# Kernel tuning notes

Hardware: AMD Instinct MI355X
Metric: run time of the kernel (lower is better)

## Reference

```python
import jax, jax.numpy as jnp
import numpy as np

DIM, NH, NL, NP, HD, FF = 256, 8, 4, 4, 32, 1024
LN_EPS = 1e-5


def _ln(x, w, b):
    m = jnp.mean(x, axis=-1, keepdims=True)
    v = jnp.mean((x - m) ** 2, axis=-1, keepdims=True)
    return (x - m) * jax.lax.rsqrt(v + LN_EPS) * w + b


def _sample_level(value_l, loc, H, W):
    # value_l: (B, H*W, nH, hd) ; loc: (B, Lq, nH, P, 2) normalized coords in [0,1]
    B, Lq, nH, P, _ = loc.shape
    # grid_sample(align_corners=False): pixel coord = norm * size - 0.5
    x = loc[..., 0] * W - 0.5
    y = loc[..., 1] * H - 0.5
    x0 = jnp.floor(x)
    y0 = jnp.floor(y)
    wx1 = x - x0
    wy1 = y - y0
    wx0 = 1.0 - wx1
    wy0 = 1.0 - wy1
    x0i = x0.astype(jnp.int32)
    y0i = y0.astype(jnp.int32)

    def corner(xi, yi, w):
        valid = ((xi >= 0) & (xi < W) & (yi >= 0) & (yi < H)).astype(value_l.dtype)
        idx = jnp.clip(yi, 0, H - 1) * W + jnp.clip(xi, 0, W - 1)
        idx = idx.transpose(0, 1, 3, 2).reshape(B, Lq * P, nH, 1)  # per-head gather index
        v = jnp.take_along_axis(value_l, idx, axis=1).reshape(B, Lq, P, nH, -1)
        wm = (w * valid).transpose(0, 1, 3, 2)[..., None]  # (B,Lq,P,nH,1)
        return v * wm

    return (corner(x0i, y0i, wx0 * wy0) + corner(x0i + 1, y0i, wx1 * wy0)
            + corner(x0i, y0i + 1, wx0 * wy1) + corner(x0i + 1, y0i + 1, wx1 * wy1))


def _msdeform_attn(q, value, ref, shapes_np, starts_np, W_off, b_off, W_attn, b_attn):
    B, S, _ = q.shape
    off = (q @ W_off + b_off).reshape(B, S, NH, NL, NP, 2)
    attn = jax.nn.softmax((q @ W_attn + b_attn).reshape(B, S, NH, NL * NP), axis=-1)
    attn = attn.reshape(B, S, NH, NL, NP)
    # offset normalizer is (W, H) per level
    norm = jnp.asarray(shapes_np[:, ::-1].copy(), dtype=q.dtype)  # (NL, 2)
    loc = ref[:, :, None, :, None, :] + off / norm[None, None, None, :, None, :]
    outs = []
    for l in range(NL):
        H, W = int(shapes_np[l, 0]), int(shapes_np[l, 1])
        s = int(starts_np[l])
        vl = value[:, s:s + H * W]  # (B, H*W, NH, HD)
        outs.append(_sample_level(vl, loc[:, :, :, l], H, W))  # (B,S,P,NH,HD)
    samp = jnp.stack(outs, axis=2)  # (B,S,NL,P,NH,HD)
    w = attn.transpose(0, 1, 3, 4, 2)[..., None]  # (B,S,NL,P,NH,1)
    return (samp * w).sum(axis=(2, 3)).reshape(B, S, NH * HD)


def setup_inputs() -> dict:
    key = jax.random.key(0)
    ks = jax.random.split(key, 16)
    shapes = np.array([[64, 64], [32, 32], [16, 16], [8, 8]], dtype=np.int64)
    starts = np.array([0, 4096, 5120, 5376], dtype=np.int64)
    B, S = 4, 5440
    std = 0.02
    return {
        "input": jax.random.normal(ks[0], (B, S, DIM), jnp.float32),
        "pos": jax.random.normal(ks[1], (B, S, DIM), jnp.float32),
        "reference_point": jax.random.uniform(ks[2], (B, S, NL, 2), jnp.float32),
        "shape": shapes,
        "level_start": starts,
        "ln1_w": jnp.ones((DIM,), jnp.float32),
        "ln1_b": jnp.zeros((DIM,), jnp.float32),
        "W_off": jax.random.normal(ks[3], (DIM, NH * NL * NP * 2), jnp.float32) * std,
        "b_off": jax.random.normal(ks[4], (NH * NL * NP * 2,), jnp.float32) * 0.1,
        "W_attn": jax.random.normal(ks[5], (DIM, NH * NL * NP), jnp.float32) * std,
        "b_attn": jnp.zeros((NH * NL * NP,), jnp.float32),
        "W_val": jax.random.normal(ks[6], (DIM, DIM), jnp.float32) * std,
        "b_val": jnp.zeros((DIM,), jnp.float32),
        "W_out": jax.random.normal(ks[7], (DIM, DIM), jnp.float32) * std,
        "b_out": jnp.zeros((DIM,), jnp.float32),
        "ln2_w": jnp.ones((DIM,), jnp.float32),
        "ln2_b": jnp.zeros((DIM,), jnp.float32),
        "ff_w1": jax.random.normal(ks[8], (DIM, FF), jnp.float32) * std,
        "ff_b1": jnp.zeros((FF,), jnp.float32),
        "ff_w2": jax.random.normal(ks[9], (FF, DIM), jnp.float32) * std,
        "ff_b2": jnp.zeros((DIM,), jnp.float32),
    }


def reference(input, pos, reference_point, shape, level_start,
              ln1_w, ln1_b, W_off, b_off, W_attn, b_attn, W_val, b_val,
              W_out, b_out, ln2_w, ln2_b, ff_w1, ff_b1, ff_w2, ff_b2):
    shapes_np = np.asarray(shape)
    starts_np = np.asarray(level_start)
    B, S, _ = input.shape
    # pre-norm query with positional embedding
    q = _ln(input, ln1_w, ln1_b) + pos
    # value projection acts on the raw residual stream (input_flatten)
    value = (input @ W_val + b_val).reshape(B, S, NH, HD)
    attn_out = _msdeform_attn(q, value, reference_point, shapes_np, starts_np,
                              W_off, b_off, W_attn, b_attn) @ W_out + b_out
    x = input + attn_out  # dropout is identity in eval
    y = _ln(x, ln2_w, ln2_b)
    ff = jax.nn.relu(y @ ff_w1 + ff_b1) @ ff_w2 + ff_b2
    return x + ff
```

## Files before the change

### kernel.cpp

```cpp
#include <hip/hip_runtime.h>
#include <hip/hip_fp16.h>
#include <math.h>

#define DIM 256
#define NHEAD 8
#define NLVL 4
#define NPT 4
#define HDIM 32
#define FFDIM 1024
#define BATCH 4
#define SEQ 5440
#define MTOK (BATCH * SEQ)

typedef __attribute__((ext_vector_type(8))) short short8;
typedef __attribute__((ext_vector_type(4))) float f32x4;

__device__ __forceinline__ unsigned short f2bf(float f) {
    union { float f; unsigned int u; } x; x.f = f;
    unsigned int r = x.u + 0x7fffu + ((x.u >> 16) & 1u);
    return (unsigned short)(r >> 16);
}

__device__ __forceinline__ void gll16(const unsigned short* g, unsigned short* l) {
    __builtin_amdgcn_global_load_lds(
        (const __attribute__((address_space(1))) void*)g,
        (__attribute__((address_space(3))) void*)l,
        16, 0, 0);
}

__global__ __launch_bounds__(256) void wtprep_kernel(
    const float* __restrict__ W_val, const float* __restrict__ W_off,
    const float* __restrict__ W_attn, const float* __restrict__ W_out,
    const float* __restrict__ ff_w1, const float* __restrict__ ff_w2,
    const float* __restrict__ b_off, const float* __restrict__ b_attn,
    unsigned short* __restrict__ wts, float* __restrict__ bcomb)
{
    int idx = blockIdx.x * 256 + threadIdx.x;
    if (blockIdx.x == 0 && threadIdx.x < 384) {
        int li = threadIdx.x;
        bcomb[li] = (li < 256) ? b_off[li] : b_attn[li - 256];
    }
    const float* W; int K, N, base;
    if      (idx < 65536)  { W = W_val;  K = 256;  N = 256;  base = 0; }
    else if (idx < 131072) { W = W_off;  K = 256;  N = 256;  base = 65536; }
    else if (idx < 163840) { W = W_attn; K = 256;  N = 128;  base = 131072; }
    else if (idx < 229376) { W = W_out;  K = 256;  N = 256;  base = 163840; }
    else if (idx < 491520) { W = ff_w1;  K = 256;  N = 1024; base = 229376; }
    else if (idx < 753664) { W = ff_w2;  K = 1024; N = 256;  base = 491520; }
    else return;
    int li = idx - base;
    int k = li % K;
    int n = li / K;
    wts[idx] = f2bf(W[(size_t)k * N + n]);
}

template<int COPY_BF16>
__global__ __launch_bounds__(256) void ln_kernel(
    const float* __restrict__ x, const float* __restrict__ w,
    const float* __restrict__ bvec, const float* __restrict__ addend,
    unsigned short* __restrict__ out, unsigned short* __restrict__ xbf)
{
    int wv = threadIdx.x >> 6, lane = threadIdx.x & 63;
    int token = blockIdx.x * 4 + wv;
    size_t base = (size_t)token * DIM + lane * 4;
    float4 v = *(const float4*)(x + base);
    float s  = v.x + v.y + v.z + v.w;
    float s2 = v.x * v.x + v.y * v.y + v.z * v.z + v.w * v.w;
    #pragma unroll
    for (int o = 1; o < 64; o <<= 1) {
        s  += __shfl_xor(s, o);
        s2 += __shfl_xor(s2, o);
    }
    float m  = s * (1.0f / DIM);
    float rs = rsqrtf(s2 * (1.0f / DIM) - m * m + 1e-5f);
    float4 w4 = *(const float4*)(w + lane * 4);
    float4 b4 = *(const float4*)(bvec + lane * 4);
    float4 r;
    r.x = (v.x - m) * rs * w4.x + b4.x;
    r.y = (v.y - m) * rs * w4.y + b4.y;
    r.z = (v.z - m) * rs * w4.z + b4.z;
    r.w = (v.w - m) * rs * w4.w + b4.w;
    if (addend) {
        float4 a = *(const float4*)(addend + base);
        r.x += a.x; r.y += a.y; r.z += a.z; r.w += a.w;
    }
    ushort4 o4;
    o4.x = f2bf(r.x); o4.y = f2bf(r.y); o4.z = f2bf(r.z); o4.w = f2bf(r.w);
    *(ushort4*)(out + base) = o4;
    if (COPY_BF16) {
        ushort4 c;
        c.x = f2bf(v.x); c.y = f2bf(v.y); c.z = f2bf(v.z); c.w = f2bf(v.w);
        *(ushort4*)(xbf + base) = c;
    }
}

template<int K, int OUT, int RELU, int HAS_RES>
__global__ __launch_bounds__(256) void mfma_gemm(
    const unsigned short* __restrict__ A,
    const unsigned short* __restrict__ Bt,
    const float* __restrict__ bias,
    const float* __restrict__ res,
    void* __restrict__ Cout,
    int M, int N)
{
    __shared__ __align__(16) unsigned short As[128 * 32];
    __shared__ __align__(16) unsigned short Bs[128 * 32];

    const int tid  = threadIdx.x;
    const int lane = tid & 63;
    const int wv   = tid >> 6;
    const int wr   = wv >> 1;
    const int wc   = wv & 1;
    const int m16  = lane & 15;
    const int quad = lane >> 4;

    const int bm0 = blockIdx.y * 128;
    const int bn0 = blockIdx.x * 128;

    const int e0 = wv * 1024 + lane * 8;
    const int e1 = e0 + 512;
    const int r0 = e0 >> 5, c0 = e0 & 31;
    const int r1 = e1 >> 5, c1 = e1 & 31;

    f32x4 acc[4][4] = {};

    for (int k0 = 0; k0 < K; k0 += 32) {
        if (k0) __syncthreads();
        gll16(A  + (size_t)(bm0 + r0) * K + k0 + c0, As + e0);
        gll16(A  + (size_t)(bm0 + r1) * K + k0 + c1, As + e1);
        gll16(Bt + (size_t)(bn0 + r0) * K + k0 + c0, Bs + e0);
        gll16(Bt + (size_t)(bn0 + r1) * K + k0 + c1, Bs + e1);
        __syncthreads();

        short8 af[4], bf[4];
        #pragma unroll
        for (int i = 0; i < 4; i++)
            af[i] = *(const short8*)&As[(wr * 64 + i * 16 + m16) * 32 + quad * 8];
        #pragma unroll
        for (int j = 0; j < 4; j++)
            bf[j] = *(const short8*)&Bs[(wc * 64 + j * 16 + m16) * 32 + quad * 8];

        #pragma unroll
        for (int i = 0; i < 4; i++)
            #pragma unroll
            for (int j = 0; j < 4; j++)
                acc[i][j] = __builtin_amdgcn_mfma_f32_16x16x32_bf16(
                    bf[j], af[i], acc[i][j], 0, 0, 0);
    }

    float4 bias4[4];
    #pragma unroll
    for (int j = 0; j < 4; j++)
        bias4[j] = *(const float4*)(bias + bn0 + wc * 64 + j * 16 + quad * 4);

    #pragma unroll
    for (int i = 0; i < 4; i++) {
        int row = bm0 + wr * 64 + i * 16 + m16;
        #pragma unroll
        for (int j = 0; j < 4; j++) {
            int col = bn0 + wc * 64 + j * 16 + quad * 4;
            float v0 = acc[i][j][0] + bias4[j].x;
            float v1 = acc[i][j][1] + bias4[j].y;
            float v2 = acc[i][j][2] + bias4[j].z;
            float v3 = acc[i][j][3] + bias4[j].w;
            if (HAS_RES) {
                float4 rr = *(const float4*)(res + (size_t)row * N + col);
                v0 += rr.x; v1 += rr.y; v2 += rr.z; v3 += rr.w;
            }
            if (RELU) {
                v0 = fmaxf(v0, 0.0f); v1 = fmaxf(v1, 0.0f);
                v2 = fmaxf(v2, 0.0f); v3 = fmaxf(v3, 0.0f);
            }
            if (OUT == 0) {
                float4 o = {v0, v1, v2, v3};
                *(float4*)((float*)Cout + (size_t)row * N + col) = o;
            } else if (OUT == 1) {
                ushort4 o;
                o.x = f2bf(v0); o.y = f2bf(v1); o.z = f2bf(v2); o.w = f2bf(v3);
                *(ushort4*)((unsigned short*)Cout + (size_t)row * N + col) = o;
            } else {
                ushort4 o;
                o.x = __half_as_ushort(__float2half_rn(v0));
                o.y = __half_as_ushort(__float2half_rn(v1));
                o.z = __half_as_ushort(__float2half_rn(v2));
                o.w = __half_as_ushort(__float2half_rn(v3));
                *(ushort4*)((unsigned short*)Cout + (size_t)row * N + col) = o;
            }
        }
    }
}

__global__ __launch_bounds__(256) void msdeform_kernel(
    const unsigned short* __restrict__ value_h,
    const float* __restrict__ oa,
    const float* __restrict__ ref,
    unsigned short* __restrict__ samp_out)
{
    const int Hs[NLVL] = {64, 32, 16, 8};
    const int Ws[NLVL] = {64, 32, 16, 8};
    const int St[NLVL] = {0, 4096, 5120, 5376};

    const int t  = threadIdx.x;
    const int tt = t >> 5;
    const int rr = t & 31;
    const int h  = rr >> 2;
    const int q  = rr & 3;
    const int token = blockIdx.x * 8 + tt;
    const int b = token / SEQ;

    __shared__ float s_attn[8][8][17];
    __shared__ uint2 s_tab[8][8][65];

    const float* oat = oa + (size_t)token * 384;
    float4 a4 = *(const float4*)(oat + 256 + h * 16 + q * 4);
    s_attn[tt][h][q * 4 + 0] = a4.x;
    s_attn[tt][h][q * 4 + 1] = a4.y;
    s_attn[tt][h][q * 4 + 2] = a4.z;
    s_attn[tt][h][q * 4 + 3] = a4.w;
    float4 o0 = *(const float4*)(oat + h * 32 + q * 8);
    float4 o1 = *(const float4*)(oat + h * 32 + q * 8 + 4);
    float2 rf = *(const float2*)(ref + (size_t)token * 8 + q * 2);
    __syncthreads();

    float mx = -1e30f;
    #pragma unroll
    for (int i = 0; i < 16; i++) mx = fmaxf(mx, s_attn[tt][h][i]);
    float sum = 0.0f;
    #pragma unroll
    for (int i = 0; i < 16; i++) sum += __expf(s_attn[tt][h][i] - mx);
    float inv = 1.0f / sum;

    {
        const int Hl = Hs[q], Wl = Ws[q], s0 = St[q];
        const float fW = (float)Wl, fH = (float)Hl;
        #pragma unroll
        for (int p = 0; p < 4; p++) {
            float ox = (p == 0) ? o0.x : (p == 1) ? o0.z : (p == 2) ? o1.x : o1.z;
            float oy = (p == 0) ? o0.y : (p == 1) ? o0.w : (p == 2) ? o1.y : o1.w;
            float aw = __expf(s_attn[tt][h][q * 4 + p] - mx) * inv;
            float x = (rf.x + ox / fW) * fW - 0.5f;
            float y = (rf.y + oy / fH) * fH - 0.5f;
            float x0f = floorf(x), y0f = floorf(y);
            float wx1 = x - x0f, wy1 = y - y0f;
            float wx0 = 1.0f - wx1, wy0 = 1.0f - wy1;
            int x0 = (int)x0f, y0 = (int)y0f;
            #pragma unroll
            for (int cy = 0; cy < 2; cy++) {
                int yi = y0 + cy;
                bool vy = (yi >= 0) && (yi < Hl);
                int yc = min(max(yi, 0), Hl - 1);
                float wy = cy ? wy1 : wy0;
                #pragma unroll
                for (int cx = 0; cx < 2; cx++) {
                    int xi = x0 + cx;
                    bool vx = (xi >= 0) && (xi < Wl);
                    int xc = min(max(xi, 0), Wl - 1);
                    float w = aw * wy * (cx ? wx1 : wx0) * ((vx && vy) ? 1.0f : 0.0f);
                    unsigned int off = (unsigned int)(s0 + yc * Wl + xc) * 512u;
                    unsigned short hw = __half_as_ushort(__float2half_rn(w));
                    unsigned int wp = (unsigned int)hw | ((unsigned int)hw << 16);
                    s_tab[tt][h][(q * 4 + p) * 4 + cy * 2 + cx] = make_uint2(off, wp);
                }
            }
        }
    }
    __syncthreads();

    const char* vb = (const char*)value_h;
    unsigned int cbase = (unsigned int)(b * (SEQ * 512)) + h * 64 + q * 16;
    const uint2* tab = &s_tab[tt][h][0];

    __half2 z; { union { unsigned int u; __half2 h; } c; c.u = 0; z = c.h; }
    __half2 acc0 = z, acc1 = z, acc2 = z, acc3 = z;

    #pragma unroll 16
    for (int i = 0; i < 64; i++) {
        uint2 e = tab[i];
        uint4 v = *(const uint4*)(vb + (cbase + e.x));
        union { unsigned int u; __half2 h; } wu; wu.u = e.y;
        union { uint4 u; __half2 h[4]; } vu; vu.u = v;
        acc0 = __hfma2(vu.h[0], wu.h, acc0);
        acc1 = __hfma2(vu.h[1], wu.h, acc1);
        acc2 = __hfma2(vu.h[2], wu.h, acc2);
        acc3 = __hfma2(vu.h[3], wu.h, acc3);
    }

    uint4 o;
    o.x = (unsigned int)f2bf(__low2float(acc0)) | ((unsigned int)f2bf(__high2float(acc0)) << 16);
    o.y = (unsigned int)f2bf(__low2float(acc1)) | ((unsigned int)f2bf(__high2float(acc1)) << 16);
    o.z = (unsigned int)f2bf(__low2float(acc2)) | ((unsigned int)f2bf(__high2float(acc2)) << 16);
    o.w = (unsigned int)f2bf(__low2float(acc3)) | ((unsigned int)f2bf(__high2float(acc3)) << 16);
    *(uint4*)(samp_out + (size_t)token * 256 + h * 32 + q * 8) = o;
}

extern "C" void kernel_launch(void* const* d_in, const int* in_sizes, int n_in,
                              void* d_out, int out_size, void* d_ws, size_t ws_size,
                              hipStream_t stream) {
    const float* input = (const float*)d_in[0];
    const float* pos   = (const float*)d_in[1];
    const float* ref   = (const float*)d_in[2];
    const float* ln1_w = (const float*)d_in[5];
    const float* ln1_b = (const float*)d_in[6];
    const float* W_off = (const float*)d_in[7];
    const float* b_off = (const float*)d_in[8];
    const float* W_attn = (const float*)d_in[9];
    const float* b_attn = (const float*)d_in[10];
    const float* W_val = (const float*)d_in[11];
    const float* b_val = (const float*)d_in[12];
    const float* W_out = (const float*)d_in[13];
    const float* b_out = (const float*)d_in[14];
    const float* ln2_w = (const float*)d_in[15];
    const float* ln2_b = (const float*)d_in[16];
    const float* ff_w1 = (const float*)d_in[17];
    const float* ff_b1 = (const float*)d_in[18];
    const float* ff_w2 = (const float*)d_in[19];
    const float* ff_b2 = (const float*)d_in[20];
    float* out = (float*)d_out;

    const size_t M = MTOK;
    float* ws = (float*)d_ws;

    unsigned short* input_bf = (unsigned short*)(ws);
    unsigned short* y_bf     = input_bf;
    unsigned short* q_bf     = (unsigned short*)(ws + M * 128);
    unsigned short* samp_bf  = q_bf;
    float*  oa_buf   = ws + M * 256;
    float*  x_buf    = oa_buf;
    unsigned short* val_h = (unsigned short*)(ws + M * 640);
    unsigned short* h_bf  = (unsigned short*)(ws + M * 768);
    unsigned short* wts   = (unsigned short*)(ws + M * 1280);
    float* bcomb = (float*)(wts + 753664);

    unsigned short* wval_t  = wts;
    unsigned short* woff_t  = wval_t  + 256 * 256;
    unsigned short* wout_t  = woff_t  + 384 * 256;
    unsigned short* ffw1_t  = wout_t  + 256 * 256;
    unsigned short* ffw2_t  = ffw1_t  + 1024 * 256;

    dim3 blk(256);

    wtprep_kernel<<<dim3(2944), blk, 0, stream>>>(
        W_val, W_off, W_attn, W_out, ff_w1, ff_w2, b_off, b_attn, wts, bcomb);

    ln_kernel<1><<<dim3(M / 4), blk, 0, stream>>>(
        input, ln1_w, ln1_b, pos, q_bf, input_bf);

    mfma_gemm<256, 2, 0, 0><<<dim3(2, M / 128), blk, 0, stream>>>(
        input_bf, wval_t, b_val, nullptr, val_h, M, 256);

    mfma_gemm<256, 0, 0, 0><<<dim3(3, M / 128), blk, 0, stream>>>(
        q_bf, woff_t, bcomb, nullptr, oa_buf, M, 384);

    msdeform_kernel<<<dim3(M / 8), blk, 0, stream>>>(
        val_h, oa_buf, ref, samp_bf);

    mfma_gemm<256, 0, 0, 1><<<dim3(2, M / 128), blk, 0, stream>>>(
        samp_bf, wout_t, b_out, input, x_buf, M, 256);

    ln_kernel<0><<<dim3(M / 4), blk, 0, stream>>>(
        x_buf, ln2_w, ln2_b, nullptr, y_bf, nullptr);

    mfma_gemm<256, 1, 1, 0><<<dim3(8, M / 128), blk, 0, stream>>>(
        y_bf, ffw1_t, ff_b1, nullptr, h_bf, M, 1024);

    mfma_gemm<1024, 0, 0, 1><<<dim3(2, M / 128), blk, 0, stream>>>(
        h_bf, ffw2_t, ff_b2, x_buf, out, M, 256);
}
```

Measured before the change: 269.7 us.

## Fuse LN1 into weight prep, merge projection GEMMs, fuse out-proj with LN2

```diff
diff --git a/kernel.cpp b/kernel.cpp
--- a/kernel.cpp
+++ b/kernel.cpp
@@ -21,24 +21,53 @@
     return (unsigned short)(r >> 16);
 }
 
-__device__ __forceinline__ void gll16(const unsigned short* g, unsigned short* l) {
-    __builtin_amdgcn_global_load_lds(
-        (const __attribute__((address_space(1))) void*)g,
-        (__attribute__((address_space(3))) void*)l,
-        16, 0, 0);
-}
-
-__global__ __launch_bounds__(256) void wtprep_kernel(
+#define LN_BLOCKS (MTOK / 4)
+
+__global__ __launch_bounds__(256) void prep_kernel(
+    const float* __restrict__ input, const float* __restrict__ pos,
+    const float* __restrict__ ln1_w, const float* __restrict__ ln1_b,
+    unsigned short* __restrict__ q_bf, unsigned short* __restrict__ input_bf,
     const float* __restrict__ W_val, const float* __restrict__ W_off,
     const float* __restrict__ W_attn, const float* __restrict__ W_out,
     const float* __restrict__ ff_w1, const float* __restrict__ ff_w2,
     const float* __restrict__ b_off, const float* __restrict__ b_attn,
     unsigned short* __restrict__ wts, float* __restrict__ bcomb)
 {
-    int idx = blockIdx.x * 256 + threadIdx.x;
-    if (blockIdx.x == 0 && threadIdx.x < 384) {
-        int li = threadIdx.x;
-        bcomb[li] = (li < 256) ? b_off[li] : b_attn[li - 256];
+    if (blockIdx.x < LN_BLOCKS) {
+        int wv = threadIdx.x >> 6, lane = threadIdx.x & 63;
+        int token = blockIdx.x * 4 + wv;
+        size_t base = (size_t)token * DIM + lane * 4;
+        float4 v = *(const float4*)(input + base);
+        float s  = v.x + v.y + v.z + v.w;
+        float s2 = v.x * v.x + v.y * v.y + v.z * v.z + v.w * v.w;
+        #pragma unroll
+        for (int o = 1; o < 64; o <<= 1) {
+            s  += __shfl_xor(s, o);
+            s2 += __shfl_xor(s2, o);
+        }
+        float m  = s * (1.0f / DIM);
+        float rs = rsqrtf(s2 * (1.0f / DIM) - m * m + 1e-5f);
+        float4 w4 = *(const float4*)(ln1_w + lane * 4);
+        float4 b4 = *(const float4*)(ln1_b + lane * 4);
+        float4 p4 = *(const float4*)(pos + base);
+        float4 r;
+        r.x = (v.x - m) * rs * w4.x + b4.x + p4.x;
+        r.y = (v.y - m) * rs * w4.y + b4.y + p4.y;
+        r.z = (v.z - m) * rs * w4.z + b4.z + p4.z;
+        r.w = (v.w - m) * rs * w4.w + b4.w + p4.w;
+        ushort4 o4;
+        o4.x = f2bf(r.x); o4.y = f2bf(r.y); o4.z = f2bf(r.z); o4.w = f2bf(r.w);
+        *(ushort4*)(q_bf + base) = o4;
+        ushort4 c;
+        c.x = f2bf(v.x); c.y = f2bf(v.y); c.z = f2bf(v.z); c.w = f2bf(v.w);
+        *(ushort4*)(input_bf + base) = c;
+        return;
+    }
+    int bidx = blockIdx.x - LN_BLOCKS;
+    int idx = bidx * 256 + threadIdx.x;
+    if (bidx == 0 && threadIdx.x < 384) {
+        bcomb[threadIdx.x] = (threadIdx.x < 256) ? b_off[threadIdx.x]
+                                                 : b_attn[threadIdx.x - 256];
     }
     const float* W; int K, N, base;
     if      (idx < 65536)  { W = W_val;  K = 256;  N = 256;  base = 0; }
@@ -54,111 +83,83 @@
     wts[idx] = f2bf(W[(size_t)k * N + n]);
 }
 
-template<int COPY_BF16>
-__global__ __launch_bounds__(256) void ln_kernel(
-    const float* __restrict__ x, const float* __restrict__ w,
-    const float* __restrict__ bvec, const float* __restrict__ addend,
-    unsigned short* __restrict__ out, unsigned short* __restrict__ xbf)
-{
-    int wv = threadIdx.x >> 6, lane = threadIdx.x & 63;
-    int token = blockIdx.x * 4 + wv;
-    size_t base = (size_t)token * DIM + lane * 4;
-    float4 v = *(const float4*)(x + base);
-    float s  = v.x + v.y + v.z + v.w;
-    float s2 = v.x * v.x + v.y * v.y + v.z * v.z + v.w * v.w;
-    #pragma unroll
-    for (int o = 1; o < 64; o <<= 1) {
-        s  += __shfl_xor(s, o);
-        s2 += __shfl_xor(s2, o);
-    }
-    float m  = s * (1.0f / DIM);
-    float rs = rsqrtf(s2 * (1.0f / DIM) - m * m + 1e-5f);
-    float4 w4 = *(const float4*)(w + lane * 4);
-    float4 b4 = *(const float4*)(bvec + lane * 4);
-    float4 r;
-    r.x = (v.x - m) * rs * w4.x + b4.x;
-    r.y = (v.y - m) * rs * w4.y + b4.y;
-    r.z = (v.z - m) * rs * w4.z + b4.z;
-    r.w = (v.w - m) * rs * w4.w + b4.w;
-    if (addend) {
-        float4 a = *(const float4*)(addend + base);
-        r.x += a.x; r.y += a.y; r.z += a.z; r.w += a.w;
-    }
-    ushort4 o4;
-    o4.x = f2bf(r.x); o4.y = f2bf(r.y); o4.z = f2bf(r.z); o4.w = f2bf(r.w);
-    *(ushort4*)(out + base) = o4;
-    if (COPY_BF16) {
-        ushort4 c;
-        c.x = f2bf(v.x); c.y = f2bf(v.y); c.z = f2bf(v.z); c.w = f2bf(v.w);
-        *(ushort4*)(xbf + base) = c;
+__device__ __forceinline__ void gemm_core(
+    const unsigned short* __restrict__ A,
+    const unsigned short* __restrict__ Bt,
+    int bm0, int bn0, int wrow, int wcol, int K,
+    int m16, int quad, f32x4 acc[4][4])
+{
+    const unsigned short* ap[4];
+    const unsigned short* bp[4];
+    #pragma unroll
+    for (int i = 0; i < 4; i++)
+        ap[i] = A + (size_t)(bm0 + wrow + i * 16 + m16) * K + quad * 8;
+    #pragma unroll
+    for (int j = 0; j < 4; j++)
+        bp[j] = Bt + (size_t)(bn0 + wcol + j * 16 + m16) * K + quad * 8;
+
+    short8 af[4], bf[4];
+    #pragma unroll
+    for (int i = 0; i < 4; i++) af[i] = *(const short8*)(ap[i]);
+    #pragma unroll
+    for (int j = 0; j < 4; j++) bf[j] = *(const short8*)(bp[j]);
+
+    #pragma unroll 2
+    for (int k0 = 0; k0 < K; k0 += 32) {
+        short8 afn[4], bfn[4];
+        if (k0 + 32 < K) {
+            #pragma unroll
+            for (int i = 0; i < 4; i++) afn[i] = *(const short8*)(ap[i] + k0 + 32);
+            #pragma unroll
+            for (int j = 0; j < 4; j++) bfn[j] = *(const short8*)(bp[j] + k0 + 32);
+        }
+        #pragma unroll
+        for (int i = 0; i < 4; i++)
+            #pragma unroll
+            for (int j = 0; j < 4; j++)
+                acc[i][j] = __builtin_amdgcn_mfma_f32_16x16x32_bf16(
+                    bf[j], af[i], acc[i][j], 0, 0, 0);
+        if (k0 + 32 < K) {
+            #pragma unroll
+            for (int i = 0; i < 4; i++) af[i] = afn[i];
+            #pragma unroll
+            for (int j = 0; j < 4; j++) bf[j] = bfn[j];
+        }
     }
 }
 
 template<int K, int OUT, int RELU, int HAS_RES>
-__global__ __launch_bounds__(256) void mfma_gemm(
+__global__ __launch_bounds__(256) void gemm_direct(
     const unsigned short* __restrict__ A,
     const unsigned short* __restrict__ Bt,
     const float* __restrict__ bias,
     const float* __restrict__ res,
-    void* __restrict__ Cout,
-    int M, int N)
-{
-    __shared__ __align__(16) unsigned short As[128 * 32];
-    __shared__ __align__(16) unsigned short Bs[128 * 32];
-
+    void* __restrict__ Cout, int N)
+{
     const int tid  = threadIdx.x;
     const int lane = tid & 63;
     const int wv   = tid >> 6;
-    const int wr   = wv >> 1;
-    const int wc   = wv & 1;
+    const int wr   = (wv >> 1) * 64;
+    const int wc   = (wv & 1) * 64;
     const int m16  = lane & 15;
     const int quad = lane >> 4;
-
     const int bm0 = blockIdx.y * 128;
     const int bn0 = blockIdx.x * 128;
 
-    const int e0 = wv * 1024 + lane * 8;
-    const int e1 = e0 + 512;
-    const int r0 = e0 >> 5, c0 = e0 & 31;
-    const int r1 = e1 >> 5, c1 = e1 & 31;
-
     f32x4 acc[4][4] = {};
-
-    for (int k0 = 0; k0 < K; k0 += 32) {
-        if (k0) __syncthreads();
-        gll16(A  + (size_t)(bm0 + r0) * K + k0 + c0, As + e0);
-        gll16(A  + (size_t)(bm0 + r1) * K + k0 + c1, As + e1);
-        gll16(Bt + (size_t)(bn0 + r0) * K + k0 + c0, Bs + e0);
-        gll16(Bt + (size_t)(bn0 + r1) * K + k0 + c1, Bs + e1);
-        __syncthreads();
-
-        short8 af[4], bf[4];
-        #pragma unroll
-        for (int i = 0; i < 4; i++)
-            af[i] = *(const short8*)&As[(wr * 64 + i * 16 + m16) * 32 + quad * 8];
-        #pragma unroll
-        for (int j = 0; j < 4; j++)
-            bf[j] = *(const short8*)&Bs[(wc * 64 + j * 16 + m16) * 32 + quad * 8];
-
-        #pragma unroll
-        for (int i = 0; i < 4; i++)
-            #pragma unroll
-            for (int j = 0; j < 4; j++)
-                acc[i][j] = __builtin_amdgcn_mfma_f32_16x16x32_bf16(
-                    bf[j], af[i], acc[i][j], 0, 0, 0);
-    }
+    gemm_core(A, Bt, bm0, bn0, wr, wc, K, m16, quad, acc);
 
     float4 bias4[4];
     #pragma unroll
     for (int j = 0; j < 4; j++)
-        bias4[j] = *(const float4*)(bias + bn0 + wc * 64 + j * 16 + quad * 4);
+        bias4[j] = *(const float4*)(bias + bn0 + wc + j * 16 + quad * 4);
 
     #pragma unroll
     for (int i = 0; i < 4; i++) {
-        int row = bm0 + wr * 64 + i * 16 + m16;
+        int row = bm0 + wr + i * 16 + m16;
         #pragma unroll
         for (int j = 0; j < 4; j++) {
-            int col = bn0 + wc * 64 + j * 16 + quad * 4;
+            int col = bn0 + wc + j * 16 + quad * 4;
             float v0 = acc[i][j][0] + bias4[j].x;
             float v1 = acc[i][j][1] + bias4[j].y;
             float v2 = acc[i][j][2] + bias4[j].z;
@@ -190,9 +191,137 @@
     }
 }
 
+__global__ __launch_bounds__(256) void gemm_dual(
+    const unsigned short* __restrict__ A0, const unsigned short* __restrict__ B0,
+    const float* __restrict__ bias0, unsigned short* __restrict__ C0,
+    const unsigned short* __restrict__ A1, const unsigned short* __restrict__ B1,
+    const float* __restrict__ bias1, unsigned short* __restrict__ C1)
+{
+    const unsigned short *A, *Bt; const float* bias; unsigned short* C;
+    int N, bx;
+    if (blockIdx.x < 2) { A = A0; Bt = B0; bias = bias0; C = C0; N = 256; bx = blockIdx.x; }
+    else                { A = A1; Bt = B1; bias = bias1; C = C1; N = 384; bx = blockIdx.x - 2; }
+
+    const int tid  = threadIdx.x;
+    const int lane = tid & 63;
+    const int wv   = tid >> 6;
+    const int wr   = (wv >> 1) * 64;
+    const int wc   = (wv & 1) * 64;
+    const int m16  = lane & 15;
+    const int quad = lane >> 4;
+    const int bm0 = blockIdx.y * 128;
+    const int bn0 = bx * 128;
+
+    f32x4 acc[4][4] = {};
+    gemm_core(A, Bt, bm0, bn0, wr, wc, 256, m16, quad, acc);
+
+    float4 bias4[4];
+    #pragma unroll
+    for (int j = 0; j < 4; j++)
+        bias4[j] = *(const float4*)(bias + bn0 + wc + j * 16 + quad * 4);
+
+    #pragma unroll
+    for (int i = 0; i < 4; i++) {
+        int row = bm0 + wr + i * 16 + m16;
+        #pragma unroll
+        for (int j = 0; j < 4; j++) {
+            int col = bn0 + wc + j * 16 + quad * 4;
+            ushort4 o;
+            o.x = __half_as_ushort(__float2half_rn(acc[i][j][0] + bias4[j].x));
+            o.y = __half_as_ushort(__float2half_rn(acc[i][j][1] + bias4[j].y));
+            o.z = __half_as_ushort(__float2half_rn(acc[i][j][2] + bias4[j].z));
+            o.w = __half_as_ushort(__float2half_rn(acc[i][j][3] + bias4[j].w));
+            *(ushort4*)(C + (size_t)row * N + col) = o;
+        }
+    }
+}
+
+__global__ __launch_bounds__(256) void gemm_ln_kernel(
+    const unsigned short* __restrict__ A,
+    const unsigned short* __restrict__ Bt,
+    const float* __restrict__ bias,
+    const float* __restrict__ res,
+    const float* __restrict__ lnw, const float* __restrict__ lnb,
+    float* __restrict__ xout, unsigned short* __restrict__ ybf)
+{
+    const int tid  = threadIdx.x;
+    const int lane = tid & 63;
+    const int wv   = tid >> 6;
+    const int m16  = lane & 15;
+    const int quad = lane >> 4;
+    const int bm0  = blockIdx.x * 64;
+    const int N = 256;
+
+    f32x4 acc[4][4] = {};
+    gemm_core(A, Bt, bm0, 0, 0, wv * 64, 256, m16, quad, acc);
+
+    float4 bias4[4], lw4[4], lb4[4];
+    #pragma unroll
+    for (int j = 0; j < 4; j++) {
+        int col = wv * 64 + j * 16 + quad * 4;
+        bias4[j] = *(const float4*)(bias + col);
+        lw4[j]   = *(const float4*)(lnw + col);
+        lb4[j]   = *(const float4*)(lnb + col);
+    }
+
+    float v[4][4][4];
+    float s1[4], s2[4];
+    #pragma unroll
+    for (int i = 0; i < 4; i++) {
+        int row = bm0 + i * 16 + m16;
+        s1[i] = 0.0f; s2[i] = 0.0f;
+        #pragma unroll
+        for (int j = 0; j < 4; j++) {
+            int col = wv * 64 + j * 16 + quad * 4;
+            float4 rr = *(const float4*)(res + (size_t)row * N + col);
+            float b0 = bias4[j].x, b1 = bias4[j].y, b2 = bias4[j].z, b3 = bias4[j].w;
+            v[i][j][0] = acc[i][j][0] + b0 + rr.x;
+            v[i][j][1] = acc[i][j][1] + b1 + rr.y;
+            v[i][j][2] = acc[i][j][2] + b2 + rr.z;
+            v[i][j][3] = acc[i][j][3] + b3 + rr.w;
+            #pragma unroll
+            for (int r = 0; r < 4; r++) {
+                s1[i] += v[i][j][r];
+                s2[i] += v[i][j][r] * v[i][j][r];
+            }
+        }
+    }
+    #pragma unroll
+    for (int i = 0; i < 4; i++) {
+        s1[i] += __shfl_xor(s1[i], 16); s1[i] += __shfl_xor(s1[i], 32);
+        s2[i] += __shfl_xor(s2[i], 16); s2[i] += __shfl_xor(s2[i], 32);
+    }
+    __shared__ float p1[4][4][16], p2[4][4][16];
+    if (quad == 0) {
+        #pragma unroll
+        for (int i = 0; i < 4; i++) { p1[wv][i][m16] = s1[i]; p2[wv][i][m16] = s2[i]; }
+    }
+    __syncthreads();
+    #pragma unroll
+    for (int i = 0; i < 4; i++) {
+        float S1 = p1[0][i][m16] + p1[1][i][m16] + p1[2][i][m16] + p1[3][i][m16];
+        float S2 = p2[0][i][m16] + p2[1][i][m16] + p2[2][i][m16] + p2[3][i][m16];
+        float m  = S1 * (1.0f / DIM);
+        float rs = rsqrtf(S2 * (1.0f / DIM) - m * m + 1e-5f);
+        int row = bm0 + i * 16 + m16;
+        #pragma unroll
+        for (int j = 0; j < 4; j++) {
+            int col = wv * 64 + j * 16 + quad * 4;
+            float4 xo = {v[i][j][0], v[i][j][1], v[i][j][2], v[i][j][3]};
+            *(float4*)(xout + (size_t)row * N + col) = xo;
+            ushort4 yo;
+            yo.x = f2bf((v[i][j][0] - m) * rs * lw4[j].x + lb4[j].x);
+            yo.y = f2bf((v[i][j][1] - m) * rs * lw4[j].y + lb4[j].y);
+            yo.z = f2bf((v[i][j][2] - m) * rs * lw4[j].z + lb4[j].z);
+            yo.w = f2bf((v[i][j][3] - m) * rs * lw4[j].w + lb4[j].w);
+            *(ushort4*)(ybf + (size_t)row * N + col) = yo;
+        }
+    }
+}
+
 __global__ __launch_bounds__(256) void msdeform_kernel(
     const unsigned short* __restrict__ value_h,
-    const float* __restrict__ oa,
+    const __half* __restrict__ oa,
     const float* __restrict__ ref,
     unsigned short* __restrict__ samp_out)
 {
@@ -211,14 +340,25 @@
     __shared__ float s_attn[8][8][17];
     __shared__ uint2 s_tab[8][8][65];
 
-    const float* oat = oa + (size_t)token * 384;
-    float4 a4 = *(const float4*)(oat + 256 + h * 16 + q * 4);
-    s_attn[tt][h][q * 4 + 0] = a4.x;
-    s_attn[tt][h][q * 4 + 1] = a4.y;
-    s_attn[tt][h][q * 4 + 2] = a4.z;
-    s_attn[tt][h][q * 4 + 3] = a4.w;
-    float4 o0 = *(const float4*)(oat + h * 32 + q * 8);
-    float4 o1 = *(const float4*)(oat + h * 32 + q * 8 + 4);
+    const __half* oat = oa + (size_t)token * 384;
+    {
+        union { uint2 u; __half2 h[2]; } au;
+        au.u = *(const uint2*)(oat + 256 + h * 16 + q * 4);
+        s_attn[tt][h][q * 4 + 0] = __low2float(au.h[0]);
+        s_attn[tt][h][q * 4 + 1] = __high2float(au.h[0]);
+        s_attn[tt][h][q * 4 + 2] = __low2float(au.h[1]);
+        s_attn[tt][h][q * 4 + 3] = __high2float(au.h[1]);
+    }
+    float ox_[4], oy_[4];
+    {
+        union { uint4 u; __half2 h[4]; } ou;
+        ou.u = *(const uint4*)(oat + h * 32 + q * 8);
+        #pragma unroll
+        for (int p = 0; p < 4; p++) {
+            ox_[p] = __low2float(ou.h[p]);
+            oy_[p] = __high2float(ou.h[p]);
+        }
+    }
     float2 rf = *(const float2*)(ref + (size_t)token * 8 + q * 2);
     __syncthreads();
 
@@ -235,11 +375,9 @@
         const float fW = (float)Wl, fH = (float)Hl;
         #pragma unroll
         for (int p = 0; p < 4; p++) {
-            float ox = (p == 0) ? o0.x : (p == 1) ? o0.z : (p == 2) ? o1.x : o1.z;
-            float oy = (p == 0) ? o0.y : (p == 1) ? o0.w : (p == 2) ? o1.y : o1.w;
             float aw = __expf(s_attn[tt][h][q * 4 + p] - mx) * inv;
-            float x = (rf.x + ox / fW) * fW - 0.5f;
-            float y = (rf.y + oy / fH) * fH - 0.5f;
+            float x = (rf.x + ox_[p] / fW) * fW - 0.5f;
+            float y = (rf.y + oy_[p] / fH) * fH - 0.5f;
             float x0f = floorf(x), y0f = floorf(y);
             float wx1 = x - x0f, wy1 = y - y0f;
             float wx0 = 1.0f - wx1, wy0 = 1.0f - wy1;
@@ -276,9 +414,9 @@
     #pragma unroll 16
     for (int i = 0; i < 64; i++) {
         uint2 e = tab[i];
-        uint4 v = *(const uint4*)(vb + (cbase + e.x));
+        uint4 vv = *(const uint4*)(vb + (cbase + e.x));
         union { unsigned int u; __half2 h; } wu; wu.u = e.y;
-        union { uint4 u; __half2 h[4]; } vu; vu.u = v;
+        union { uint4 u; __half2 h[4]; } vu; vu.u = vv;
         acc0 = __hfma2(vu.h[0], wu.h, acc0);
         acc1 = __hfma2(vu.h[1], wu.h, acc1);
         acc2 = __hfma2(vu.h[2], wu.h, acc2);
@@ -324,11 +462,11 @@
     unsigned short* y_bf     = input_bf;
     unsigned short* q_bf     = (unsigned short*)(ws + M * 128);
     unsigned short* samp_bf  = q_bf;
-    float*  oa_buf   = ws + M * 256;
-    float*  x_buf    = oa_buf;
-    unsigned short* val_h = (unsigned short*)(ws + M * 640);
-    unsigned short* h_bf  = (unsigned short*)(ws + M * 768);
-    unsigned short* wts   = (unsigned short*)(ws + M * 1280);
+    __half* oa_h  = (__half*)(ws + M * 256);
+    float*  x_buf = ws + M * 448;
+    unsigned short* val_h = (unsigned short*)(ws + M * 704);
+    unsigned short* h_bf  = (unsigned short*)(ws + M * 832);
+    unsigned short* wts   = (unsigned short*)(ws + M * 1344);
     float* bcomb = (float*)(wts + 753664);
 
     unsigned short* wval_t  = wts;
@@ -339,30 +477,23 @@
 
     dim3 blk(256);
 
-    wtprep_kernel<<<dim3(2944), blk, 0, stream>>>(
+    prep_kernel<<<dim3(LN_BLOCKS + 2944), blk, 0, stream>>>(
+        input, pos, ln1_w, ln1_b, q_bf, input_bf,
         W_val, W_off, W_attn, W_out, ff_w1, ff_w2, b_off, b_attn, wts, bcomb);
 
-    ln_kernel<1><<<dim3(M / 4), blk, 0, stream>>>(
-        input, ln1_w, ln1_b, pos, q_bf, input_bf);
-
-    mfma_gemm<256, 2, 0, 0><<<dim3(2, M / 128), blk, 0, stream>>>(
-        input_bf, wval_t, b_val, nullptr, val_h, M, 256);
-
-    mfma_gemm<256, 0, 0, 0><<<dim3(3, M / 128), blk, 0, stream>>>(
-        q_bf, woff_t, bcomb, nullptr, oa_buf, M, 384);
+    gemm_dual<<<dim3(5, M / 128), blk, 0, stream>>>(
+        input_bf, wval_t, b_val, (unsigned short*)val_h,
+        q_bf, woff_t, bcomb, (unsigned short*)oa_h);
 
     msdeform_kernel<<<dim3(M / 8), blk, 0, stream>>>(
-        val_h, oa_buf, ref, samp_bf);
-
-    mfma_gemm<256, 0, 0, 1><<<dim3(2, M / 128), blk, 0, stream>>>(
-        samp_bf, wout_t, b_out, input, x_buf, M, 256);
-
-    ln_kernel<0><<<dim3(M / 4), blk, 0, stream>>>(
-        x_buf, ln2_w, ln2_b, nullptr, y_bf, nullptr);
-
-    mfma_gemm<256, 1, 1, 0><<<dim3(8, M / 128), blk, 0, stream>>>(
-        y_bf, ffw1_t, ff_b1, nullptr, h_bf, M, 1024);
-
-    mfma_gemm<1024, 0, 0, 1><<<dim3(2, M / 128), blk, 0, stream>>>(
-        h_bf, ffw2_t, ff_b2, x_buf, out, M, 256);
-}
+        val_h, oa_h, ref, samp_bf);
+
+    gemm_ln_kernel<<<dim3(M / 64), blk, 0, stream>>>(
+        samp_bf, wout_t, b_out, input, ln2_w, ln2_b, x_buf, y_bf);
+
+    gemm_direct<256, 1, 1, 0><<<dim3(8, M / 128), blk, 0, stream>>>(
+        y_bf, ffw1_t, ff_b1, nullptr, h_bf, 1024);
+
+    gemm_direct<1024, 0, 0, 1><<<dim3(2, M / 128), blk, 0, stream>>>(
+        h_bf, ffw2_t, ff_b2, x_buf, out, 256);
+}
```

Result: slower. 341.5 us (+26.6%).
